# Kernel tuning notes

Measured on AMD Instinct MI355X. Metric: run time of the kernel, lower is better.

The kernel has to match this reference:

```python
import jax, jax.numpy as jnp
import numpy as np

DIM = 768
HEADS = 12
HEAD_DIM = DIM // HEADS
SCALE = HEAD_DIM ** (-0.5)


def setup_inputs() -> dict:
    key = jax.random.key(0)
    k1, k2, k3, k4 = jax.random.split(key, 4)
    B, N = 16, 4096
    rgb_tokens = jax.random.normal(k1, (B, N, DIM), dtype=jnp.float32)
    depth_tokens = jax.random.normal(k2, (B, N, DIM), dtype=jnp.float32)
    # nn.Linear(dim, 2*dim, bias=False): store as [dim, 2*dim] for x @ W
    w_std = 1.0 / np.sqrt(DIM)
    W_kv_rgb = jax.random.uniform(k3, (DIM, 2 * DIM), dtype=jnp.float32, minval=-w_std, maxval=w_std)
    W_kv_depth = jax.random.uniform(k4, (DIM, 2 * DIM), dtype=jnp.float32, minval=-w_std, maxval=w_std)
    return {"rgb_tokens": rgb_tokens, "depth_tokens": depth_tokens,
            "W_kv_rgb": W_kv_rgb, "W_kv_depth": W_kv_depth}


def _split_heads(x):
    # [B, N, C] -> [B, H, N, hd]
    B, N, C = x.shape
    return x.reshape(B, N, HEADS, HEAD_DIM).transpose(0, 2, 1, 3)


def _kv(x, W):
    B, N, C = x.shape
    kv = (x @ W).reshape(B, N, 2, HEADS, HEAD_DIM)
    kv = kv.transpose(2, 0, 3, 1, 4)  # [2, B, H, N, hd]
    return kv[0], kv[1]


def _ctx(k, v):
    # K^T @ V context: [B, H, hd, hd], softmax over the first hd axis (dim=-2)
    ctx = jnp.einsum('bhnd,bhne->bhde', k, v) * SCALE
    return jax.nn.softmax(ctx, axis=-2)


def reference(rgb_tokens, depth_tokens, W_kv_rgb, W_kv_depth):
    B, N, C = rgb_tokens.shape
    q_rgb = _split_heads(rgb_tokens)
    q_depth = _split_heads(depth_tokens)
    k_rgb, v_rgb = _kv(rgb_tokens, W_kv_rgb)
    k_depth, v_depth = _kv(depth_tokens, W_kv_depth)
    ctx_rgb = _ctx(k_rgb, v_rgb)
    ctx_depth = _ctx(k_depth, v_depth)
    rgb_out = jnp.einsum('bhnd,bhde->bhne', q_rgb, ctx_depth)
    depth_out = jnp.einsum('bhnd,bhde->bhne', q_depth, ctx_rgb)
    rgb_out = rgb_out.transpose(0, 2, 1, 3).reshape(B, N, C)
    depth_out = depth_out.transpose(0, 2, 1, 3).reshape(B, N, C)
    return (rgb_out, depth_out)
```

## Files before the change

kernel.cpp:

```cpp
#include <hip/hip_runtime.h>
#include <hip/hip_bf16.h>

#define BB 16
#define NN 4096
#define CC 768
#define HH 12
#define HD 64
#define SCALE_F 0.125f

typedef unsigned short u16;
typedef unsigned int u32;
typedef __bf16 bf16x8 __attribute__((ext_vector_type(8)));
typedef float f32x4 __attribute__((ext_vector_type(4)));
typedef u16 u16x4 __attribute__((ext_vector_type(4)));

__device__ __forceinline__ u16 f2bf(float f) {
  union { __hip_bfloat16 h; u16 u; } v;
  v.h = __float2bfloat16(f);
  return v.u;
}

__device__ __forceinline__ float bf2f(u16 u) {
  union { unsigned int i; float f; } v;
  v.i = ((unsigned int)u) << 16;
  return v.f;
}

__device__ __forceinline__ void split2(float f, u16& hi, u16& lo) {
  hi = f2bf(f);
  lo = f2bf(f - bf2f(hi));
}

__device__ __forceinline__ f32x4 mfma16(bf16x8 a, bf16x8 b, f32x4 c) {
  return __builtin_amdgcn_mfma_f32_16x16x32_bf16(a, b, c, 0, 0, 0);
}

union bfr_u { bf16x8 v; u16 u[8]; };

__device__ __forceinline__ void load_split8(const float* p, bf16x8& hi, bf16x8& lo) {
  f32x4 v0 = *(const f32x4*)p;
  f32x4 v1 = *(const f32x4*)(p + 4);
  bfr_u h, l;
  for (int i = 0; i < 4; i++) split2(v0[i], h.u[i], l.u[i]);
  for (int i = 0; i < 4; i++) split2(v1[i], h.u[4 + i], l.u[4 + i]);
  hi = h.v; lo = l.v;
}

__device__ __forceinline__ void gl_lds16(const u16* gsrc, u16* ldst) {
  __builtin_amdgcn_global_load_lds(
      (const __attribute__((address_space(1))) u32*)gsrc,
      (__attribute__((address_space(3))) u32*)ldst, 16, 0, 0);
}

__global__ __launch_bounds__(256) void xcast_kernel(const float* __restrict__ x0,
                                                    const float* __restrict__ x1,
                                                    u16* __restrict__ Xb) {
  const size_t total = (size_t)BB * NN * CC;
  const float* X = blockIdx.y ? x1 : x0;
  u16* O = Xb + (size_t)blockIdx.y * total;
  size_t i = ((size_t)blockIdx.x * 256 + threadIdx.x) * 8;
  const size_t step = (size_t)gridDim.x * 256 * 8;
  for (; i < total; i += step) {
    f32x4 a = *(const f32x4*)(X + i);
    f32x4 b = *(const f32x4*)(X + i + 4);
    bfr_u h;
    for (int j = 0; j < 4; j++) h.u[j] = f2bf(a[j]);
    for (int j = 0; j < 4; j++) h.u[4 + j] = f2bf(b[j]);
    *(bf16x8*)&O[i] = h.v;
  }
}

__global__ __launch_bounds__(256) void wtrans_kernel(const float* __restrict__ w0,
                                                     const float* __restrict__ w1,
                                                     u16* __restrict__ WTh,
                                                     u16* __restrict__ WTl) {
  __shared__ float tile[64][65];
  const float* W = blockIdx.z ? w1 : w0;
  const size_t obase = (size_t)blockIdx.z * (1536 * 768);
  const int col0 = blockIdx.x * 64;
  const int c0   = blockIdx.y * 64;
  const int t = threadIdx.x;
  const int lc = t & 63;
  const int lr = t >> 6;
  for (int r = lr; r < 64; r += 4)
    tile[r][lc] = W[(size_t)(c0 + r) * 1536 + col0 + lc];
  __syncthreads();
  for (int r = lr; r < 64; r += 4) {
    u16 hi, lo;
    split2(tile[lc][r], hi, lo);
    WTh[obase + (size_t)(col0 + r) * CC + c0 + lc] = hi;
    WTl[obase + (size_t)(col0 + r) * CC + c0 + lc] = lo;
  }
}

__device__ __forceinline__ int gtile_addr(int c, int k) {
  return (c >> 2) * 168 + (c & 3) * 8 + (k >> 3) * 32 + (k & 7);
}

__global__ __launch_bounds__(256) void gram_kernel(const u16* __restrict__ Xb,
                                                   u16* __restrict__ Gh,
                                                   u16* __restrict__ Gl) {
  __shared__ u16 As[32 * 168];
  __shared__ u16 Bs[32 * 168];

  const int dd = blockIdx.x;
  const int j = dd >> 3;
  const int g = (j / 21) * 8 + (dd & 7);
  int idx = j % 21;
  const int b = g & 15, modal = g >> 4;

  int ti = 0;
  while (idx >= 6 - ti) { idx -= 6 - ti; ti++; }
  const int tj = ti + idx;
  const u16* X = Xb + (size_t)(modal * BB + b) * NN * CC;
  const size_t goff = (size_t)(modal * BB + b) * CC * CC;
  u16* Ghb = Gh + goff;
  u16* Glb = Gl + goff;

  const int t = threadIdx.x;
  const int lane = t & 63;
  const int w = t >> 6;
  const int lm = lane & 15;
  const int q = lane >> 4;
  const int wm = (w & 1) * 64;
  const int wn = (w >> 1) * 64;

  const bool diag = (ti == tj);

  const int tt = t & 127;
  const int sc0 = (tt & 15) * 8;
  const int snb = (tt >> 4) * 4;
  const bool isB = (t >= 128);
  const int tile0 = (isB ? tj : ti) * 128;
  u16* T = isB ? Bs : As;
  const bool do_stage = !(isB && diag);

  f32x4 acc[4][4];
  for (int i = 0; i < 4; i++)
    for (int jj = 0; jj < 4; jj++) { f32x4 z = {0.f, 0.f, 0.f, 0.f}; acc[i][jj] = z; }

  for (int kc = 0; kc < NN / 32; kc++) {
    const int n0 = kc * 32;
    __syncthreads();
    if (do_stage) {
      const u16* src = X + (size_t)(n0 + snb) * CC + tile0 + sc0;
      bfr_u r0, r1, r2, r3;
      r0.v = *(const bf16x8*)(src);
      r1.v = *(const bf16x8*)(src + CC);
      r2.v = *(const bf16x8*)(src + 2 * CC);
      r3.v = *(const bf16x8*)(src + 3 * CC);
#pragma unroll
      for (int i = 0; i < 8; i++) {
        u16x4 p = {r0.u[i], r1.u[i], r2.u[i], r3.u[i]};
        *(u16x4*)&T[gtile_addr(sc0 + i, snb)] = p;
      }
    }
    __syncthreads();
    const u16* Bp = diag ? As : Bs;
    bf16x8 af[4], bfr[4];
    for (int mt = 0; mt < 4; mt++)
      af[mt] = *(const bf16x8*)&As[gtile_addr(wm + mt * 16 + lm, q * 8)];
    for (int nt = 0; nt < 4; nt++)
      bfr[nt] = *(const bf16x8*)&Bp[gtile_addr(wn + nt * 16 + lm, q * 8)];
    for (int mt = 0; mt < 4; mt++)
      for (int nt = 0; nt < 4; nt++)
        acc[mt][nt] = mfma16(af[mt], bfr[nt], acc[mt][nt]);
  }

  for (int mt = 0; mt < 4; mt++)
    for (int nt = 0; nt < 4; nt++) {
      const int row0 = ti * 128 + wm + mt * 16 + q * 4;
      const int col  = tj * 128 + wn + nt * 16 + lm;
      f32x4 v = acc[mt][nt];
      u16 hi[4], lo[4];
      for (int i = 0; i < 4; i++) split2(v[i], hi[i], lo[i]);
      for (int i = 0; i < 4; i++) {
        Ghb[(size_t)(row0 + i) * CC + col] = hi[i];
        Glb[(size_t)(row0 + i) * CC + col] = lo[i];
      }
      if (!diag) {
        u16x4 ph = {hi[0], hi[1], hi[2], hi[3]};
        u16x4 pl = {lo[0], lo[1], lo[2], lo[3]};
        *(u16x4*)&Ghb[(size_t)col * CC + row0] = ph;
        *(u16x4*)&Glb[(size_t)col * CC + row0] = pl;
      }
    }
}

__global__ __launch_bounds__(256) void ctx1_kernel(const u16* __restrict__ WTh,
                                                   const u16* __restrict__ WTl,
                                                   const u16* __restrict__ Gh,
                                                   const u16* __restrict__ Gl,
                                                   float* __restrict__ UT) {
  __shared__ __align__(16) u16 lds[32768];

  const int dd = blockIdx.x;
  const int j = dd >> 3;
  const int g = (j / 36) * 8 + (dd & 7);
  const int i = j % 36;
  const int b = g & 15, modal = g >> 4;
  const int ti = i / 6, tj = i % 6;

  const size_t goff = (size_t)(modal * BB + b) * CC * CC;
  const u16* Ghb = Gh + goff;
  const u16* Glb = Gl + goff;
  const int vbase = modal * 1536 + 768 + tj * 128;
  float* UTb = UT + (size_t)(modal * BB + b) * CC * CC;

  const int t = threadIdx.x;
  const int lane = t & 63, w = t >> 6;
  const int lm = lane & 15, q = lane >> 4;
  const int wm = (w & 1) * 64, wn = (w >> 1) * 64;

  const int srow = lane >> 3;
  const int sg = (lane & 7) ^ srow;
  const u16* comp_src;
  if (w < 2) comp_src = (w == 0 ? Ghb : Glb) + (size_t)(ti * 128 + srow) * CC + sg * 8;
  else       comp_src = (w == 2 ? WTh : WTl) + (size_t)(vbase + srow) * CC + sg * 8;
  u16* comp_dst = &lds[w * 8192];

  f32x4 acc[4][4];
  for (int mt = 0; mt < 4; mt++)
    for (int nt = 0; nt < 4; nt++) { f32x4 z = {0.f, 0.f, 0.f, 0.f}; acc[mt][nt] = z; }

  for (int kc = 0; kc < 12; kc++) {
    __syncthreads();
#pragma unroll
    for (int ii = 0; ii < 16; ii++)
      gl_lds16(comp_src + (size_t)ii * 8 * CC + kc * 64, comp_dst + ii * 512);
    __syncthreads();
#pragma unroll
    for (int kk = 0; kk < 2; kk++) {
      bf16x8 ah[4], al_[4], bh[4], bl_[4];
      const int gq8 = ((kk * 4 + q) ^ (lm & 7)) * 8;
#pragma unroll
      for (int mt = 0; mt < 4; mt++) {
        const int ro = (wm + mt * 16 + lm) * 64;
        ah[mt]  = *(const bf16x8*)&lds[ro + gq8];
        al_[mt] = *(const bf16x8*)&lds[8192 + ro + gq8];
      }
#pragma unroll
      for (int nt = 0; nt < 4; nt++) {
        const int ro = (wn + nt * 16 + lm) * 64;
        bh[nt]  = *(const bf16x8*)&lds[16384 + ro + gq8];
        bl_[nt] = *(const bf16x8*)&lds[24576 + ro + gq8];
      }
#pragma unroll
      for (int mt = 0; mt < 4; mt++)
#pragma unroll
        for (int nt = 0; nt < 4; nt++) {
          acc[mt][nt] = mfma16(ah[mt], bh[nt], acc[mt][nt]);
          acc[mt][nt] = mfma16(al_[mt], bh[nt], acc[mt][nt]);
          acc[mt][nt] = mfma16(ah[mt], bl_[nt], acc[mt][nt]);
        }
    }
  }

  for (int mt = 0; mt < 4; mt++)
    for (int nt = 0; nt < 4; nt++) {
      const int e = tj * 128 + wn + nt * 16 + lm;
      const int r0 = ti * 128 + wm + mt * 16 + q * 4;
      *(f32x4*)&UTb[(size_t)e * CC + r0] = acc[mt][nt];
    }
}

__global__ __launch_bounds__(256) void ctx2_kernel(const u16* __restrict__ WTh,
                                                   const u16* __restrict__ WTl,
                                                   const float* __restrict__ UT,
                                                   u16* __restrict__ ctxT) {
  __shared__ float cs[64 * 68];
  const int h = blockIdx.x, b = blockIdx.y, modal = blockIdx.z;
  const float* UTb = UT + (size_t)(modal * BB + b) * CC * CC;
  const size_t krow = (size_t)modal * 1536 + h * HD;
  u16* cout = ctxT + ((size_t)((modal * BB + b) * HH + h)) * (HD * HD);

  const int t = threadIdx.x;
  const int lane = t & 63, w = t >> 6;
  const int lm = lane & 15, q = lane >> 4;
  const int d0 = w * 16;

  f32x4 acc[4];
  for (int i = 0; i < 4; i++) { f32x4 z = {0.f, 0.f, 0.f, 0.f}; acc[i] = z; }

  const u16* akh = &WTh[(krow + d0 + lm) * CC];
  const u16* akl = &WTl[(krow + d0 + lm) * CC];
  const float* ub = &UTb[(size_t)(h * HD) * CC];
  for (int rc = 0; rc < 24; rc++) {
    const int co = rc * 32 + q * 8;
    bf16x8 ah = *(const bf16x8*)&akh[co];
    bf16x8 al = *(const bf16x8*)&akl[co];
#pragma unroll
    for (int nt = 0; nt < 4; nt++) {
      bf16x8 bh, bl;
      load_split8(&ub[(size_t)(nt * 16 + lm) * CC + co], bh, bl);
      acc[nt] = mfma16(ah, bh, acc[nt]);
      acc[nt] = mfma16(al, bh, acc[nt]);
      acc[nt] = mfma16(ah, bl, acc[nt]);
    }
  }
  for (int nt = 0; nt < 4; nt++) {
    const int e = nt * 16 + lm;
    for (int i = 0; i < 4; i++)
      cs[(d0 + q * 4 + i) * 68 + e] = acc[nt][i] * SCALE_F;
  }
  __syncthreads();
  if (t < 64) {
    const int e = t;
    float mx = -1e30f;
    for (int d = 0; d < 64; d++) mx = fmaxf(mx, cs[d * 68 + e]);
    float s = 0.f;
    for (int d = 0; d < 64; d++) s += __expf(cs[d * 68 + e] - mx);
    const float inv = 1.f / s;
    for (int d = 0; d < 64; d++)
      cout[e * 64 + d] = f2bf(__expf(cs[d * 68 + e] - mx) * inv);
  }
}

__global__ __launch_bounds__(256) void ctx_kernel(const u16* __restrict__ WTh,
                                                  const u16* __restrict__ WTl,
                                                  const u16* __restrict__ Gh,
                                                  const u16* __restrict__ Gl,
                                                  u16* __restrict__ ctxT) {
  __shared__ __align__(16) float Us[64 * 196];
  float* cs = Us;

  const int h = blockIdx.x, b = blockIdx.y, modal = blockIdx.z;
  const size_t goff = (size_t)(modal * BB + b) * CC * CC;
  const u16* Ghb = Gh + goff;
  const u16* Glb = Gl + goff;
  const size_t vrow = (size_t)modal * 1536 + 768 + h * HD;
  const size_t krow = (size_t)modal * 1536 + h * HD;
  u16* cout = ctxT + ((size_t)((modal * BB + b) * HH + h)) * (HD * HD);

  const int t = threadIdx.x;
  const int lane = t & 63, w = t >> 6;
  const int lm = lane & 15, q = lane >> 4;
  const int d0 = w * 16;

  f32x4 acc2[4];
  for (int i = 0; i < 4; i++) { f32x4 z = {0.f, 0.f, 0.f, 0.f}; acc2[i] = z; }

  for (int p = 0; p < 4; p++) {
    const int rbase = p * 192;
    __syncthreads();
    for (int mi = 0; mi < 3; mi++) {
      const int row0 = w * 48 + mi * 16;
      const size_t r = (size_t)(rbase + row0 + lm) * CC;
      f32x4 acc[4];
      for (int i = 0; i < 4; i++) { f32x4 z = {0.f, 0.f, 0.f, 0.f}; acc[i] = z; }
      for (int kc = 0; kc < 24; kc++) {
        const int co = kc * 32 + q * 8;
        bf16x8 ah = *(const bf16x8*)&Ghb[r + co];
        bf16x8 al = *(const bf16x8*)&Glb[r + co];
        for (int nt = 0; nt < 4; nt++) {
          bf16x8 bh = *(const bf16x8*)&WTh[(vrow + nt * 16 + lm) * CC + co];
          bf16x8 bl = *(const bf16x8*)&WTl[(vrow + nt * 16 + lm) * CC + co];
          acc[nt] = mfma16(ah, bh, acc[nt]);
          acc[nt] = mfma16(al, bh, acc[nt]);
          acc[nt] = mfma16(ah, bl, acc[nt]);
        }
      }
      for (int nt = 0; nt < 4; nt++)
        *(f32x4*)&Us[(nt * 16 + lm) * 196 + row0 + q * 4] = acc[nt];
    }
    __syncthreads();
    for (int rc = 0; rc < 6; rc++) {
      bf16x8 ah = *(const bf16x8*)&WTh[(krow + d0 + lm) * CC + rbase + rc * 32 + q * 8];
      bf16x8 al = *(const bf16x8*)&WTl[(krow + d0 + lm) * CC + rbase + rc * 32 + q * 8];
      for (int nt = 0; nt < 4; nt++) {
        bf16x8 bh, bl;
        load_split8(&Us[(nt * 16 + lm) * 196 + rc * 32 + q * 8], bh, bl);
        acc2[nt] = mfma16(ah, bh, acc2[nt]);
        acc2[nt] = mfma16(al, bh, acc2[nt]);
        acc2[nt] = mfma16(ah, bl, acc2[nt]);
      }
    }
  }
  __syncthreads();
  for (int nt = 0; nt < 4; nt++) {
    const int e = nt * 16 + lm;
    for (int i = 0; i < 4; i++)
      cs[(d0 + q * 4 + i) * 68 + e] = acc2[nt][i] * SCALE_F;
  }
  __syncthreads();
  if (t < 64) {
    const int e = t;
    float mx = -1e30f;
    for (int d = 0; d < 64; d++) mx = fmaxf(mx, cs[d * 68 + e]);
    float s = 0.f;
    for (int d = 0; d < 64; d++) s += __expf(cs[d * 68 + e] - mx);
    const float inv = 1.f / s;
    for (int d = 0; d < 64; d++)
      cout[e * 64 + d] = f2bf(__expf(cs[d * 68 + e] - mx) * inv);
  }
}

__global__ __launch_bounds__(256) void out_kernel(const u16* __restrict__ Xb,
                                                  const u16* __restrict__ ctxT,
                                                  float* __restrict__ out) {
  __shared__ u16 Xs[32 * 776];
  const int nt0 = blockIdx.x;
  const int b = blockIdx.y, modal = blockIdx.z;
  const u16* X = Xb + (size_t)(modal * BB + b) * NN * CC + (size_t)nt0 * 32 * CC;
  const u16* ctxb = ctxT + (size_t)(((modal ^ 1) * BB + b) * HH) * (HD * HD);
  float* O = out + (size_t)modal * BB * NN * CC + (size_t)b * NN * CC + (size_t)nt0 * 32 * CC;

  const int t = threadIdx.x;
  for (int idx = t; idx < 32 * 96; idx += 256) {
    const int r = idx / 96, c8 = idx % 96;
    *(bf16x8*)&Xs[r * 776 + c8 * 8] = *(const bf16x8*)&X[(size_t)r * CC + c8 * 8];
  }
  __syncthreads();

  const int lane = t & 63, w = t >> 6;
  const int lm = lane & 15, q = lane >> 4;
  const int mt = w & 1;
  const int hh = (w >> 1) * 6;
  for (int hi = 0; hi < 6; hi++) {
    const int h = hh + hi;
    bf16x8 a0 = *(const bf16x8*)&Xs[(mt * 16 + lm) * 776 + h * 64 + 0 + q * 8];
    bf16x8 a1 = *(const bf16x8*)&Xs[(mt * 16 + lm) * 776 + h * 64 + 32 + q * 8];
    const u16* ch = ctxb + (size_t)h * (HD * HD);
    for (int et = 0; et < 4; et++) {
      f32x4 acc = {0.f, 0.f, 0.f, 0.f};
      bf16x8 b0 = *(const bf16x8*)&ch[(et * 16 + lm) * 64 + 0 + q * 8];
      bf16x8 b1 = *(const bf16x8*)&ch[(et * 16 + lm) * 64 + 32 + q * 8];
      acc = mfma16(a0, b0, acc);
      acc = mfma16(a1, b1, acc);
      for (int i = 0; i < 4; i++)
        O[(size_t)(mt * 16 + q * 4 + i) * CC + h * 64 + et * 16 + lm] = acc[i];
    }
  }
}

extern "C" void kernel_launch(void* const* d_in, const int* in_sizes, int n_in,
                              void* d_out, int out_size, void* d_ws, size_t ws_size,
                              hipStream_t stream) {
  (void)in_sizes; (void)n_in; (void)out_size;
  const float* rgb   = (const float*)d_in[0];
  const float* dep   = (const float*)d_in[1];
  const float* w_rgb = (const float*)d_in[2];
  const float* w_dep = (const float*)d_in[3];
  float* out = (float*)d_out;

  char* ws = (char*)d_ws;
  u16* WTh = (u16*)ws;
  u16* WTl = (u16*)(ws + 4718592);
  u16* Gh  = (u16*)(ws + 9437184);
  u16* Gl  = (u16*)(ws + 47185920);
  u16* CT  = (u16*)(ws + 84934656);
  u16* Xbf = (u16*)(ws + 88080384);
  const size_t UT_OFF = 289406976ull;
  const size_t WS_NEED = UT_OFF + 75497472ull;

  xcast_kernel<<<dim3(4096, 2), 256, 0, stream>>>(rgb, dep, Xbf);
  wtrans_kernel<<<dim3(24, 12, 2), 256, 0, stream>>>(w_rgb, w_dep, WTh, WTl);
  gram_kernel<<<dim3(672, 1, 1), 256, 0, stream>>>(Xbf, Gh, Gl);
  if (ws_size >= WS_NEED) {
    float* UT = (float*)(ws + UT_OFF);
    ctx1_kernel<<<dim3(1152, 1, 1), 256, 0, stream>>>(WTh, WTl, Gh, Gl, UT);
    ctx2_kernel<<<dim3(HH, BB, 2), 256, 0, stream>>>(WTh, WTl, UT, CT);
  } else {
    ctx_kernel<<<dim3(HH, BB, 2), 256, 0, stream>>>(WTh, WTl, Gh, Gl, CT);
  }
  out_kernel<<<dim3(128, BB, 2), 256, 0, stream>>>(Xbf, CT, out);
}
```

Before: 1.158 ms.

## Store bf16 tokens transposed and stage Gram tiles via direct global-to-LDS loads

```diff
diff --git a/kernel.cpp b/kernel.cpp
--- a/kernel.cpp
+++ b/kernel.cpp
@@ -37,37 +37,29 @@
 
 union bfr_u { bf16x8 v; u16 u[8]; };
 
-__device__ __forceinline__ void load_split8(const float* p, bf16x8& hi, bf16x8& lo) {
-  f32x4 v0 = *(const f32x4*)p;
-  f32x4 v1 = *(const f32x4*)(p + 4);
-  bfr_u h, l;
-  for (int i = 0; i < 4; i++) split2(v0[i], h.u[i], l.u[i]);
-  for (int i = 0; i < 4; i++) split2(v1[i], h.u[4 + i], l.u[4 + i]);
-  hi = h.v; lo = l.v;
-}
-
 __device__ __forceinline__ void gl_lds16(const u16* gsrc, u16* ldst) {
   __builtin_amdgcn_global_load_lds(
       (const __attribute__((address_space(1))) u32*)gsrc,
       (__attribute__((address_space(3))) u32*)ldst, 16, 0, 0);
 }
 
-__global__ __launch_bounds__(256) void xcast_kernel(const float* __restrict__ x0,
-                                                    const float* __restrict__ x1,
-                                                    u16* __restrict__ Xb) {
-  const size_t total = (size_t)BB * NN * CC;
-  const float* X = blockIdx.y ? x1 : x0;
-  u16* O = Xb + (size_t)blockIdx.y * total;
-  size_t i = ((size_t)blockIdx.x * 256 + threadIdx.x) * 8;
-  const size_t step = (size_t)gridDim.x * 256 * 8;
-  for (; i < total; i += step) {
-    f32x4 a = *(const f32x4*)(X + i);
-    f32x4 b = *(const f32x4*)(X + i + 4);
-    bfr_u h;
-    for (int j = 0; j < 4; j++) h.u[j] = f2bf(a[j]);
-    for (int j = 0; j < 4; j++) h.u[4 + j] = f2bf(b[j]);
-    *(bf16x8*)&O[i] = h.v;
-  }
+__global__ __launch_bounds__(256) void xcastT_kernel(const float* __restrict__ x0,
+                                                     const float* __restrict__ x1,
+                                                     u16* __restrict__ XbT) {
+  __shared__ float tile[64][65];
+  const int z = blockIdx.z;
+  const int b = z & 15, modal = z >> 4;
+  const float* X = (modal ? x1 : x0) + (size_t)b * NN * CC;
+  u16* O = XbT + (size_t)z * CC * NN;
+  const int n0 = blockIdx.x * 64;
+  const int c0 = blockIdx.y * 64;
+  const int t = threadIdx.x;
+  const int lc = t & 63, lr = t >> 6;
+  for (int r = lr; r < 64; r += 4)
+    tile[r][lc] = X[(size_t)(n0 + r) * CC + c0 + lc];
+  __syncthreads();
+  for (int r = lr; r < 64; r += 4)
+    O[(size_t)(c0 + r) * NN + n0 + lc] = f2bf(tile[lc][r]);
 }
 
 __global__ __launch_bounds__(256) void wtrans_kernel(const float* __restrict__ w0,
@@ -93,15 +85,11 @@
   }
 }
 
-__device__ __forceinline__ int gtile_addr(int c, int k) {
-  return (c >> 2) * 168 + (c & 3) * 8 + (k >> 3) * 32 + (k & 7);
-}
-
-__global__ __launch_bounds__(256) void gram_kernel(const u16* __restrict__ Xb,
+__global__ __launch_bounds__(256) void gram_kernel(const u16* __restrict__ XbT,
                                                    u16* __restrict__ Gh,
                                                    u16* __restrict__ Gl) {
-  __shared__ u16 As[32 * 168];
-  __shared__ u16 Bs[32 * 168];
+  __shared__ __align__(16) u16 As[128 * 64];
+  __shared__ __align__(16) u16 Bs[128 * 64];
 
   const int dd = blockIdx.x;
   const int j = dd >> 3;
@@ -112,7 +100,9 @@
   int ti = 0;
   while (idx >= 6 - ti) { idx -= 6 - ti; ti++; }
   const int tj = ti + idx;
-  const u16* X = Xb + (size_t)(modal * BB + b) * NN * CC;
+  const bool diag = (ti == tj);
+
+  const u16* Xbm = XbT + (size_t)(modal * BB + b) * CC * NN;
   const size_t goff = (size_t)(modal * BB + b) * CC * CC;
   u16* Ghb = Gh + goff;
   u16* Glb = Gl + goff;
@@ -125,46 +115,46 @@
   const int wm = (w & 1) * 64;
   const int wn = (w >> 1) * 64;
 
-  const bool diag = (ti == tj);
-
-  const int tt = t & 127;
-  const int sc0 = (tt & 15) * 8;
-  const int snb = (tt >> 4) * 4;
-  const bool isB = (t >= 128);
-  const int tile0 = (isB ? tj : ti) * 128;
-  u16* T = isB ? Bs : As;
-  const bool do_stage = !(isB && diag);
+  const int srow = lane >> 3;
+  const int skg = (lane & 7) ^ srow;
+  const u16* srcA = Xbm + (size_t)(ti * 128 + w * 32 + srow) * NN + skg * 8;
+  const u16* srcB = Xbm + (size_t)(tj * 128 + w * 32 + srow) * NN + skg * 8;
+  u16* dstA = &As[(w * 32) * 64];
+  u16* dstB = &Bs[(w * 32) * 64];
 
   f32x4 acc[4][4];
   for (int i = 0; i < 4; i++)
     for (int jj = 0; jj < 4; jj++) { f32x4 z = {0.f, 0.f, 0.f, 0.f}; acc[i][jj] = z; }
 
-  for (int kc = 0; kc < NN / 32; kc++) {
-    const int n0 = kc * 32;
+  for (int kc = 0; kc < NN / 64; kc++) {
+    const int k0 = kc * 64;
     __syncthreads();
-    if (do_stage) {
-      const u16* src = X + (size_t)(n0 + snb) * CC + tile0 + sc0;
-      bfr_u r0, r1, r2, r3;
-      r0.v = *(const bf16x8*)(src);
-      r1.v = *(const bf16x8*)(src + CC);
-      r2.v = *(const bf16x8*)(src + 2 * CC);
-      r3.v = *(const bf16x8*)(src + 3 * CC);
-#pragma unroll
-      for (int i = 0; i < 8; i++) {
-        u16x4 p = {r0.u[i], r1.u[i], r2.u[i], r3.u[i]};
-        *(u16x4*)&T[gtile_addr(sc0 + i, snb)] = p;
-      }
+#pragma unroll
+    for (int ii = 0; ii < 4; ii++)
+      gl_lds16(srcA + (size_t)ii * 8 * NN + k0, dstA + ii * 512);
+    if (!diag) {
+#pragma unroll
+      for (int ii = 0; ii < 4; ii++)
+        gl_lds16(srcB + (size_t)ii * 8 * NN + k0, dstB + ii * 512);
     }
     __syncthreads();
     const u16* Bp = diag ? As : Bs;
-    bf16x8 af[4], bfr[4];
-    for (int mt = 0; mt < 4; mt++)
-      af[mt] = *(const bf16x8*)&As[gtile_addr(wm + mt * 16 + lm, q * 8)];
-    for (int nt = 0; nt < 4; nt++)
-      bfr[nt] = *(const bf16x8*)&Bp[gtile_addr(wn + nt * 16 + lm, q * 8)];
-    for (int mt = 0; mt < 4; mt++)
+#pragma unroll
+    for (int kk = 0; kk < 2; kk++) {
+      bf16x8 af[4], bfr[4];
+      const int gq8 = ((kk * 4 + q) ^ (lm & 7)) * 8;
+#pragma unroll
+      for (int mt = 0; mt < 4; mt++)
+        af[mt] = *(const bf16x8*)&As[(wm + mt * 16 + lm) * 64 + gq8];
+#pragma unroll
       for (int nt = 0; nt < 4; nt++)
-        acc[mt][nt] = mfma16(af[mt], bfr[nt], acc[mt][nt]);
+        bfr[nt] = *(const bf16x8*)&Bp[(wn + nt * 16 + lm) * 64 + gq8];
+#pragma unroll
+      for (int mt = 0; mt < 4; mt++)
+#pragma unroll
+        for (int nt = 0; nt < 4; nt++)
+          acc[mt][nt] = mfma16(af[mt], bfr[nt], acc[mt][nt]);
+    }
   }
 
   for (int mt = 0; mt < 4; mt++)
@@ -191,7 +181,8 @@
                                                    const u16* __restrict__ WTl,
                                                    const u16* __restrict__ Gh,
                                                    const u16* __restrict__ Gl,
-                                                   float* __restrict__ UT) {
+                                                   u16* __restrict__ UTh,
+                                                   u16* __restrict__ UTl) {
   __shared__ __align__(16) u16 lds[32768];
 
   const int dd = blockIdx.x;
@@ -205,7 +196,7 @@
   const u16* Ghb = Gh + goff;
   const u16* Glb = Gl + goff;
   const int vbase = modal * 1536 + 768 + tj * 128;
-  float* UTb = UT + (size_t)(modal * BB + b) * CC * CC;
+  const size_t uoff = (size_t)(modal * BB + b) * CC * CC;
 
   const int t = threadIdx.x;
   const int lane = t & 63, w = t >> 6;
@@ -260,17 +251,26 @@
     for (int nt = 0; nt < 4; nt++) {
       const int e = tj * 128 + wn + nt * 16 + lm;
       const int r0 = ti * 128 + wm + mt * 16 + q * 4;
-      *(f32x4*)&UTb[(size_t)e * CC + r0] = acc[mt][nt];
+      f32x4 v = acc[mt][nt];
+      u16 hi[4], lo[4];
+      for (int ii = 0; ii < 4; ii++) split2(v[ii], hi[ii], lo[ii]);
+      u16x4 ph = {hi[0], hi[1], hi[2], hi[3]};
+      u16x4 pl = {lo[0], lo[1], lo[2], lo[3]};
+      *(u16x4*)&UTh[uoff + (size_t)e * CC + r0] = ph;
+      *(u16x4*)&UTl[uoff + (size_t)e * CC + r0] = pl;
     }
 }
 
 __global__ __launch_bounds__(256) void ctx2_kernel(const u16* __restrict__ WTh,
                                                    const u16* __restrict__ WTl,
-                                                   const float* __restrict__ UT,
+                                                   const u16* __restrict__ UTh,
+                                                   const u16* __restrict__ UTl,
                                                    u16* __restrict__ ctxT) {
   __shared__ float cs[64 * 68];
   const int h = blockIdx.x, b = blockIdx.y, modal = blockIdx.z;
-  const float* UTb = UT + (size_t)(modal * BB + b) * CC * CC;
+  const size_t uoff = (size_t)(modal * BB + b) * CC * CC;
+  const u16* Uh = UTh + uoff + (size_t)(h * HD) * CC;
+  const u16* Ul = UTl + uoff + (size_t)(h * HD) * CC;
   const size_t krow = (size_t)modal * 1536 + h * HD;
   u16* cout = ctxT + ((size_t)((modal * BB + b) * HH + h)) * (HD * HD);
 
@@ -284,15 +284,14 @@
 
   const u16* akh = &WTh[(krow + d0 + lm) * CC];
   const u16* akl = &WTl[(krow + d0 + lm) * CC];
-  const float* ub = &UTb[(size_t)(h * HD) * CC];
   for (int rc = 0; rc < 24; rc++) {
     const int co = rc * 32 + q * 8;
     bf16x8 ah = *(const bf16x8*)&akh[co];
     bf16x8 al = *(const bf16x8*)&akl[co];
 #pragma unroll
     for (int nt = 0; nt < 4; nt++) {
-      bf16x8 bh, bl;
-      load_split8(&ub[(size_t)(nt * 16 + lm) * CC + co], bh, bl);
+      bf16x8 bh = *(const bf16x8*)&Uh[(size_t)(nt * 16 + lm) * CC + co];
+      bf16x8 bl = *(const bf16x8*)&Ul[(size_t)(nt * 16 + lm) * CC + co];
       acc[nt] = mfma16(ah, bh, acc[nt]);
       acc[nt] = mfma16(al, bh, acc[nt]);
       acc[nt] = mfma16(ah, bl, acc[nt]);
@@ -316,99 +315,23 @@
   }
 }
 
-__global__ __launch_bounds__(256) void ctx_kernel(const u16* __restrict__ WTh,
-                                                  const u16* __restrict__ WTl,
-                                                  const u16* __restrict__ Gh,
-                                                  const u16* __restrict__ Gl,
-                                                  u16* __restrict__ ctxT) {
-  __shared__ __align__(16) float Us[64 * 196];
-  float* cs = Us;
-
-  const int h = blockIdx.x, b = blockIdx.y, modal = blockIdx.z;
-  const size_t goff = (size_t)(modal * BB + b) * CC * CC;
-  const u16* Ghb = Gh + goff;
-  const u16* Glb = Gl + goff;
-  const size_t vrow = (size_t)modal * 1536 + 768 + h * HD;
-  const size_t krow = (size_t)modal * 1536 + h * HD;
-  u16* cout = ctxT + ((size_t)((modal * BB + b) * HH + h)) * (HD * HD);
-
-  const int t = threadIdx.x;
-  const int lane = t & 63, w = t >> 6;
-  const int lm = lane & 15, q = lane >> 4;
-  const int d0 = w * 16;
-
-  f32x4 acc2[4];
-  for (int i = 0; i < 4; i++) { f32x4 z = {0.f, 0.f, 0.f, 0.f}; acc2[i] = z; }
-
-  for (int p = 0; p < 4; p++) {
-    const int rbase = p * 192;
-    __syncthreads();
-    for (int mi = 0; mi < 3; mi++) {
-      const int row0 = w * 48 + mi * 16;
-      const size_t r = (size_t)(rbase + row0 + lm) * CC;
-      f32x4 acc[4];
-      for (int i = 0; i < 4; i++) { f32x4 z = {0.f, 0.f, 0.f, 0.f}; acc[i] = z; }
-      for (int kc = 0; kc < 24; kc++) {
-        const int co = kc * 32 + q * 8;
-        bf16x8 ah = *(const bf16x8*)&Ghb[r + co];
-        bf16x8 al = *(const bf16x8*)&Glb[r + co];
-        for (int nt = 0; nt < 4; nt++) {
-          bf16x8 bh = *(const bf16x8*)&WTh[(vrow + nt * 16 + lm) * CC + co];
-          bf16x8 bl = *(const bf16x8*)&WTl[(vrow + nt * 16 + lm) * CC + co];
-          acc[nt] = mfma16(ah, bh, acc[nt]);
-          acc[nt] = mfma16(al, bh, acc[nt]);
-          acc[nt] = mfma16(ah, bl, acc[nt]);
-        }
-      }
-      for (int nt = 0; nt < 4; nt++)
-        *(f32x4*)&Us[(nt * 16 + lm) * 196 + row0 + q * 4] = acc[nt];
-    }
-    __syncthreads();
-    for (int rc = 0; rc < 6; rc++) {
-      bf16x8 ah = *(const bf16x8*)&WTh[(krow + d0 + lm) * CC + rbase + rc * 32 + q * 8];
-      bf16x8 al = *(const bf16x8*)&WTl[(krow + d0 + lm) * CC + rbase + rc * 32 + q * 8];
-      for (int nt = 0; nt < 4; nt++) {
-        bf16x8 bh, bl;
-        load_split8(&Us[(nt * 16 + lm) * 196 + rc * 32 + q * 8], bh, bl);
-        acc2[nt] = mfma16(ah, bh, acc2[nt]);
-        acc2[nt] = mfma16(al, bh, acc2[nt]);
-        acc2[nt] = mfma16(ah, bl, acc2[nt]);
-      }
-    }
-  }
-  __syncthreads();
-  for (int nt = 0; nt < 4; nt++) {
-    const int e = nt * 16 + lm;
-    for (int i = 0; i < 4; i++)
-      cs[(d0 + q * 4 + i) * 68 + e] = acc2[nt][i] * SCALE_F;
-  }
-  __syncthreads();
-  if (t < 64) {
-    const int e = t;
-    float mx = -1e30f;
-    for (int d = 0; d < 64; d++) mx = fmaxf(mx, cs[d * 68 + e]);
-    float s = 0.f;
-    for (int d = 0; d < 64; d++) s += __expf(cs[d * 68 + e] - mx);
-    const float inv = 1.f / s;
-    for (int d = 0; d < 64; d++)
-      cout[e * 64 + d] = f2bf(__expf(cs[d * 68 + e] - mx) * inv);
-  }
-}
-
-__global__ __launch_bounds__(256) void out_kernel(const u16* __restrict__ Xb,
+__global__ __launch_bounds__(256) void out_kernel(const float* __restrict__ x0,
+                                                  const float* __restrict__ x1,
                                                   const u16* __restrict__ ctxT,
                                                   float* __restrict__ out) {
   __shared__ u16 Xs[32 * 776];
   const int nt0 = blockIdx.x;
   const int b = blockIdx.y, modal = blockIdx.z;
-  const u16* X = Xb + (size_t)(modal * BB + b) * NN * CC + (size_t)nt0 * 32 * CC;
+  const float* X = (modal ? x1 : x0) + (size_t)b * NN * CC + (size_t)nt0 * 32 * CC;
   const u16* ctxb = ctxT + (size_t)(((modal ^ 1) * BB + b) * HH) * (HD * HD);
   float* O = out + (size_t)modal * BB * NN * CC + (size_t)b * NN * CC + (size_t)nt0 * 32 * CC;
 
   const int t = threadIdx.x;
-  for (int idx = t; idx < 32 * 96; idx += 256) {
-    const int r = idx / 96, c8 = idx % 96;
-    *(bf16x8*)&Xs[r * 776 + c8 * 8] = *(const bf16x8*)&X[(size_t)r * CC + c8 * 8];
+  for (int idx = t; idx < 32 * 192; idx += 256) {
+    const int r = idx / 192, cq = idx % 192;
+    float4 v = *(const float4*)&X[(size_t)r * CC + cq * 4];
+    u16x4 pk = {f2bf(v.x), f2bf(v.y), f2bf(v.z), f2bf(v.w)};
+    *(u16x4*)&Xs[r * 776 + cq * 4] = pk;
   }
   __syncthreads();
 
@@ -436,7 +359,7 @@
 extern "C" void kernel_launch(void* const* d_in, const int* in_sizes, int n_in,
                               void* d_out, int out_size, void* d_ws, size_t ws_size,
                               hipStream_t stream) {
-  (void)in_sizes; (void)n_in; (void)out_size;
+  (void)in_sizes; (void)n_in; (void)out_size; (void)ws_size;
   const float* rgb   = (const float*)d_in[0];
   const float* dep   = (const float*)d_in[1];
   const float* w_rgb = (const float*)d_in[2];
@@ -449,19 +372,14 @@
   u16* Gh  = (u16*)(ws + 9437184);
   u16* Gl  = (u16*)(ws + 47185920);
   u16* CT  = (u16*)(ws + 84934656);
-  u16* Xbf = (u16*)(ws + 88080384);
-  const size_t UT_OFF = 289406976ull;
-  const size_t WS_NEED = UT_OFF + 75497472ull;
-
-  xcast_kernel<<<dim3(4096, 2), 256, 0, stream>>>(rgb, dep, Xbf);
+  u16* XbT = (u16*)(ws + 88080384);
+  u16* UTh = (u16*)(ws + 289406976);
+  u16* UTl = (u16*)(ws + 327155712);
+
+  xcastT_kernel<<<dim3(64, 12, 32), 256, 0, stream>>>(rgb, dep, XbT);
   wtrans_kernel<<<dim3(24, 12, 2), 256, 0, stream>>>(w_rgb, w_dep, WTh, WTl);
-  gram_kernel<<<dim3(672, 1, 1), 256, 0, stream>>>(Xbf, Gh, Gl);
-  if (ws_size >= WS_NEED) {
-    float* UT = (float*)(ws + UT_OFF);
-    ctx1_kernel<<<dim3(1152, 1, 1), 256, 0, stream>>>(WTh, WTl, Gh, Gl, UT);
-    ctx2_kernel<<<dim3(HH, BB, 2), 256, 0, stream>>>(WTh, WTl, UT, CT);
-  } else {
-    ctx_kernel<<<dim3(HH, BB, 2), 256, 0, stream>>>(WTh, WTl, Gh, Gl, CT);
-  }
-  out_kernel<<<dim3(128, BB, 2), 256, 0, stream>>>(Xbf, CT, out);
-}
+  gram_kernel<<<dim3(672, 1, 1), 256, 0, stream>>>(XbT, Gh, Gl);
+  ctx1_kernel<<<dim3(1152, 1, 1), 256, 0, stream>>>(WTh, WTl, Gh, Gl, UTh, UTl);
+  ctx2_kernel<<<dim3(HH, BB, 2), 256, 0, stream>>>(WTh, WTl, UTh, UTl, CT);
+  out_kernel<<<dim3(128, BB, 2), 256, 0, stream>>>(rgb, dep, CT, out);
+}
```

Result: faster. 1.131 ms (-2.3%).
